# Optimization experiments

Measured on AMD Instinct MI355X. Metric: run time of the kernel, lower is better.

## Reference

```python
import jax, jax.numpy as jnp
import numpy as np

D_MODEL = 1024
D_INNER = 2048
D_STATE = 16
D_CONV = 4
DT_RANK = 64
BATCH = 2
SEQLEN = 1024


def setup_inputs() -> dict:
    key = jax.random.key(0)
    ks = jax.random.split(key, 12)
    s = 0.02
    # dt bias initialized as inverse-softplus of dt ~ LogUniform(1e-3, 1e-1), as in the torch code
    dt = jnp.exp(jax.random.uniform(ks[7], (D_INNER,)) * (np.log(0.1) - np.log(0.001)) + np.log(0.001))
    dt = jnp.clip(dt, 1e-4, None)
    inv_dt = jnp.log(jnp.expm1(dt))
    A_log = jnp.log(jnp.broadcast_to(jnp.arange(1, D_STATE + 1, dtype=jnp.float32), (D_INNER, D_STATE)))
    return {
        "hidden_states": jax.random.normal(ks[0], (BATCH, SEQLEN, D_MODEL), jnp.float32),
        "x_text": jax.random.normal(ks[1], (BATCH, D_MODEL), jnp.float32),
        "in_proj_w": jax.random.normal(ks[2], (2 * D_INNER, D_MODEL), jnp.float32) * s,
        "conv_w": jax.random.normal(ks[3], (D_INNER, 1, D_CONV), jnp.float32) * s,
        "conv_b": jax.random.normal(ks[4], (D_INNER,), jnp.float32) * s,
        "x_proj_w": jax.random.normal(ks[5], (DT_RANK + 2 * D_STATE, D_INNER), jnp.float32) * s,
        "dt_proj_w": jax.random.normal(ks[6], (D_INNER, DT_RANK), jnp.float32) * (DT_RANK ** -0.5),
        "dt_proj_b": inv_dt.astype(jnp.float32),
        "A_log": A_log.astype(jnp.float32),
        "D": jnp.ones((D_INNER,), jnp.float32),
        "out_proj_w": jax.random.normal(ks[8], (D_MODEL, D_INNER), jnp.float32) * s,
        "gate_w": jax.random.normal(ks[9], (DT_RANK + 2 * D_STATE, D_MODEL), jnp.float32) * s,
        "gate_b": jnp.zeros((DT_RANK + 2 * D_STATE,), jnp.float32),
    }


def _causal_depthwise_conv(x, w, b):
    # x: (b, d, l), w: (d, 1, k) depthwise, left-pad k-1 for causality
    y = jax.lax.conv_general_dilated(
        x, w, window_strides=(1,), padding=[(D_CONV - 1, 0)],
        dimension_numbers=("NCH", "OIH", "NCH"), feature_group_count=D_INNER)
    return y + b[None, :, None]


def _mamba_forward(hidden_states, x_text, in_proj_w, conv_w, conv_b, x_proj_w,
                   dt_proj_w, dt_proj_b, A_log, D, out_proj_w, gate_w, gate_b):
    b = hidden_states.shape[0]
    # input projection -> x, z each (b, l, d_inner)
    xz = jnp.einsum("bld,ed->ble", hidden_states, in_proj_w)
    x, z = jnp.split(xz, 2, axis=-1)
    # causal depthwise conv + SiLU
    xc = _causal_depthwise_conv(jnp.transpose(x, (0, 2, 1)), conv_w, conv_b)
    xc = jnp.transpose(jax.nn.silu(xc), (0, 2, 1))  # (b, l, d_inner)
    # x_proj -> dt/B/C, modulated by text gate
    x_dbl = jnp.einsum("bld,ed->ble", xc, x_proj_w)  # (b, l, dt_rank+2n)
    gate = jax.nn.sigmoid(x_text @ gate_w.T + gate_b)  # (b, dt_rank+2n)
    x_dbl = x_dbl * gate[:, None, :]
    dt, Bm, Cm = jnp.split(x_dbl, [DT_RANK, DT_RANK + D_STATE], axis=-1)
    delta = jax.nn.softplus(jnp.einsum("blr,dr->bld", dt, dt_proj_w) + dt_proj_b)  # (b, l, d)
    A = -jnp.exp(A_log)  # (d, n)
    dA = jnp.exp(jnp.einsum("bld,dn->bldn", delta, A))          # (b, l, d, n)
    dBx = jnp.einsum("bld,bln->bldn", delta * xc, Bm)            # (b, l, d, n)

    def step(h, inp):
        dA_t, dBx_t, C_t = inp
        h = h * dA_t + dBx_t                       # (b, d, n)
        y_t = jnp.einsum("bdn,bn->bd", h, C_t)
        return h, y_t

    h0 = jnp.zeros((b, D_INNER, D_STATE), delta.dtype)
    _, ys = jax.lax.scan(step, h0, (jnp.transpose(dA, (1, 0, 2, 3)),
                                    jnp.transpose(dBx, (1, 0, 2, 3)),
                                    jnp.transpose(Cm, (1, 0, 2))))
    y = jnp.transpose(ys, (1, 0, 2)) + D * xc      # (b, l, d_inner)
    y = y * jax.nn.silu(z)
    return jnp.einsum("bld,md->blm", y, out_proj_w)


def reference(hidden_states, x_text, in_proj_w, conv_w, conv_b, x_proj_w,
              dt_proj_w, dt_proj_b, A_log, D, out_proj_w, gate_w, gate_b):
    return _mamba_forward(hidden_states, x_text, in_proj_w, conv_w, conv_b, x_proj_w,
                          dt_proj_w, dt_proj_b, A_log, D, out_proj_w, gate_w, gate_b)
```

## Files before the change

### kernel.cpp

```cpp
#include <hip/hip_runtime.h>

#define BATCH   2
#define SEQLEN  1024
#define DMODEL  1024
#define DINNER  2048
#define DSTATE  16
#define DCONV   4
#define DTRANK  64
#define GDIM    96
#define MROWS   (BATCH*SEQLEN)

#define NCHUNK  64
#define LCHUNK  16
#define SPLITX  16
#define SPLITO  2

typedef __attribute__((ext_vector_type(8))) short bf16x8_t;
typedef __attribute__((ext_vector_type(4))) float f32x4_t;
typedef __attribute__((ext_vector_type(4))) unsigned short u16x4_t;
typedef unsigned short ushort_t;

__device__ __forceinline__ unsigned short f2bf(float x) {
    union { float f; unsigned int u; } v; v.f = x;
    unsigned int r = v.u + 0x7FFFu + ((v.u >> 16) & 1u);
    return (unsigned short)(r >> 16);
}
__device__ __forceinline__ float bf2f(unsigned short h) {
    union { unsigned int u; float f; } v; v.u = ((unsigned int)h) << 16;
    return v.f;
}

__device__ __forceinline__ void gload_lds16(const ushort_t* g, short* l) {
    __builtin_amdgcn_global_load_lds(
        (const __attribute__((address_space(1))) unsigned int*)g,
        (__attribute__((address_space(3))) unsigned int*)l, 16, 0, 0);
}

#define N1 (MROWS*DMODEL)
#define N2 (2*DINNER*DMODEL)
#define N3 (GDIM*DINNER)
#define N4 (DINNER*DTRANK)
#define N5 (DMODEL*DINNER)
#define NTOT (N1+N2+N3+N4+N5)
__global__ __launch_bounds__(256)
void cvt5_kernel(const float* __restrict__ s1, const float* __restrict__ s2,
                 const float* __restrict__ s3, const float* __restrict__ s4,
                 const float* __restrict__ s5,
                 ushort_t* o1, ushort_t* o2, ushort_t* o3, ushort_t* o4, ushort_t* o5) {
    int idx = (blockIdx.x * 256 + threadIdx.x) * 4;
    if (idx >= NTOT) return;
    const float* src; ushort_t* dst;
    if (idx < N1)              { src = s1; dst = o1; }
    else if ((idx -= N1) < N2) { src = s2; dst = o2; }
    else if ((idx -= N2) < N3) { src = s3; dst = o3; }
    else if ((idx -= N3) < N4) { src = s4; dst = o4; }
    else                       { idx -= N4; src = s5; dst = o5; }
    f32x4_t v = *(const f32x4_t*)(src + idx);
    u16x4_t o;
    #pragma unroll
    for (int j = 0; j < 4; j++) o[j] = f2bf(v[j]);
    *(u16x4_t*)(dst + idx) = o;
}

template<int EPI>
__global__ __launch_bounds__(256)
void gemm_bf(const ushort_t* __restrict__ A, const ushort_t* __restrict__ W,
             void* __restrict__ out0, void* __restrict__ out1,
             const float* __restrict__ bias, int M, int N, int K) {
    __shared__ __align__(16) short As[2][128 * 32];
    __shared__ __align__(16) short Bs[2][128 * 32];

    const int tid  = threadIdx.x;
    const int m0   = blockIdx.x * 128;
    const int n0   = blockIdx.y * 128;
    const int klen = K / gridDim.z;
    const int kbeg = blockIdx.z * klen;

    const int w    = tid >> 6;
    const int lane = tid & 63;
    const int quad = lane >> 4;
    const int l15  = lane & 15;
    const int wm   = (w >> 1) * 64;
    const int wn   = (w & 1) * 64;

    const int rA0 = (w * 2 + 0) * 16 + (lane >> 2);
    const int rA1 = (w * 2 + 1) * 16 + (lane >> 2);
    const int kc  = (((lane & 3) ^ ((lane >> 3) & 3)) << 3);
    const int arow0 = m0 + rA0;
    const int arow1 = m0 + rA1;
    int brow0 = n0 + rA0; if (brow0 > N - 1) brow0 = N - 1;
    int brow1 = n0 + rA1; if (brow1 > N - 1) brow1 = N - 1;

    const int sw = ((quad ^ ((l15 >> 1) & 3)) << 3);

    f32x4_t acc[4][4];
    #pragma unroll
    for (int i = 0; i < 4; i++)
        #pragma unroll
        for (int j = 0; j < 4; j++)
            acc[i][j] = (f32x4_t){0.f, 0.f, 0.f, 0.f};

    {
        const int kk = kbeg + kc;
        gload_lds16(A + (size_t)arow0 * K + kk, &As[0][(w * 2 + 0) * 512]);
        gload_lds16(A + (size_t)arow1 * K + kk, &As[0][(w * 2 + 1) * 512]);
        gload_lds16(W + (size_t)brow0 * K + kk, &Bs[0][(w * 2 + 0) * 512]);
        gload_lds16(W + (size_t)brow1 * K + kk, &Bs[0][(w * 2 + 1) * 512]);
    }

    int cur = 0;
    for (int k0 = 0; k0 < klen; k0 += 32) {
        if (k0 + 32 < klen) {
            const int kk = kbeg + k0 + 32 + kc;
            gload_lds16(A + (size_t)arow0 * K + kk, &As[cur ^ 1][(w * 2 + 0) * 512]);
            gload_lds16(A + (size_t)arow1 * K + kk, &As[cur ^ 1][(w * 2 + 1) * 512]);
            gload_lds16(W + (size_t)brow0 * K + kk, &Bs[cur ^ 1][(w * 2 + 0) * 512]);
            gload_lds16(W + (size_t)brow1 * K + kk, &Bs[cur ^ 1][(w * 2 + 1) * 512]);
            asm volatile("s_waitcnt vmcnt(4)" ::: "memory");
        } else {
            asm volatile("s_waitcnt vmcnt(0)" ::: "memory");
        }
        __builtin_amdgcn_sched_barrier(0);
        asm volatile("s_barrier" ::: "memory");
        __builtin_amdgcn_sched_barrier(0);

        bf16x8_t af[4], bfv[4];
        #pragma unroll
        for (int mi = 0; mi < 4; mi++)
            af[mi] = *(const bf16x8_t*)(&As[cur][(wm + mi * 16 + l15) * 32 + sw]);
        #pragma unroll
        for (int ni = 0; ni < 4; ni++)
            bfv[ni] = *(const bf16x8_t*)(&Bs[cur][(wn + ni * 16 + l15) * 32 + sw]);
        #pragma unroll
        for (int mi = 0; mi < 4; mi++)
            #pragma unroll
            for (int ni = 0; ni < 4; ni++)
                acc[mi][ni] = __builtin_amdgcn_mfma_f32_16x16x32_bf16(af[mi], bfv[ni], acc[mi][ni], 0, 0, 0);

        __builtin_amdgcn_sched_barrier(0);
        asm volatile("s_barrier" ::: "memory");
        __builtin_amdgcn_sched_barrier(0);
        cur ^= 1;
    }

    const size_t zoff = (size_t)blockIdx.z * M * N;
    #pragma unroll
    for (int mi = 0; mi < 4; mi++) {
        #pragma unroll
        for (int ni = 0; ni < 4; ni++) {
            #pragma unroll
            for (int r = 0; r < 4; r++) {
                int gm = m0 + wm + mi * 16 + quad * 4 + r;
                int gn = n0 + wn + ni * 16 + l15;
                if (gn < N) {
                    float v = acc[mi][ni][r];
                    if (EPI == 0) {
                        ((float*)out0)[zoff + (size_t)gm * N + gn] = v;
                    } else if (EPI == 1) {
                        float t = v + bias[gn];
                        float sp = (t > 20.f) ? t : log1pf(__expf(t));
                        ((ushort_t*)out0)[(size_t)gm * N + gn] = f2bf(sp);
                    } else {
                        if (gn < DINNER)
                            ((float*)out0)[(size_t)gm * DINNER + gn] = v;
                        else
                            ((float*)out1)[(size_t)gm * DINNER + (gn - DINNER)] = v;
                    }
                }
            }
        }
    }
}

#define CONVBLK ((MROWS*DINNER)/256)
__global__ __launch_bounds__(256)
void convgate_kernel(const float* __restrict__ x,
                     const float* __restrict__ cw,
                     const float* __restrict__ cb,
                     ushort_t* __restrict__ xc,
                     const float* __restrict__ xt,
                     const float* __restrict__ gw,
                     const float* __restrict__ gb,
                     float* __restrict__ gate) {
    if (blockIdx.x < CONVBLK) {
        int idx = blockIdx.x * 256 + threadIdx.x;
        int d  = idx & (DINNER - 1);
        int bl = idx >> 11;
        int l  = bl & (SEQLEN - 1);
        float acc = cb[d];
        #pragma unroll
        for (int j = 0; j < DCONV; j++) {
            int lj = l - (DCONV - 1) + j;
            if (lj >= 0)
                acc += cw[d * DCONV + j] * x[(size_t)(bl - (DCONV - 1) + j) * DINNER + d];
        }
        float v = acc / (1.f + __expf(-acc));
        xc[idx] = f2bf(v);
    } else {
        int g = blockIdx.x - CONVBLK;
        int b = g / GDIM, j = g % GDIM;
        int tid = threadIdx.x;
        float s = 0.f;
        for (int k = tid; k < DMODEL; k += 256)
            s += xt[b * DMODEL + k] * gw[j * DMODEL + k];
        #pragma unroll
        for (int o = 32; o > 0; o >>= 1) s += __shfl_down(s, o);
        __shared__ float red[4];
        if ((tid & 63) == 0) red[tid >> 6] = s;
        __syncthreads();
        if (tid == 0) {
            float t = red[0] + red[1] + red[2] + red[3] + gb[j];
            gate[b * GDIM + j] = 1.f / (1.f + __expf(-t));
        }
    }
}

__global__ void gatemul_kernel(const float* __restrict__ xp,
                               const float* __restrict__ gate,
                               ushort_t* __restrict__ dt,
                               float* __restrict__ Bm,
                               float* __restrict__ Cm) {
    int idx = blockIdx.x * 256 + threadIdx.x;
    if (idx >= MROWS * GDIM) return;
    int j  = idx % GDIM;
    int bl = idx / GDIM;
    int b  = bl >> 10;
    float v = 0.f;
    #pragma unroll
    for (int z = 0; z < SPLITX; z++)
        v += xp[(size_t)z * MROWS * GDIM + idx];
    v *= gate[b * GDIM + j];
    if (j < DTRANK)               dt[bl * DTRANK + j] = f2bf(v);
    else if (j < DTRANK + DSTATE) Bm[bl * DSTATE + (j - DTRANK)] = v;
    else                          Cm[bl * DSTATE + (j - DTRANK - DSTATE)] = v;
}

__global__ __launch_bounds__(256)
void scan1_kernel(const ushort_t* __restrict__ delta,
                  const ushort_t* __restrict__ xc,
                  const float* __restrict__ Bm,
                  const float* __restrict__ A_log,
                  float* __restrict__ hfin,
                  float* __restrict__ dsum) {
    __shared__ float sBm[LCHUNK][DSTATE];
    int tid = threadIdx.x;
    int d = blockIdx.x * 256 + tid;
    int b = blockIdx.y;
    int c = blockIdx.z;
    int l0 = c * LCHUNK;
    for (int t = tid; t < LCHUNK * DSTATE; t += 256)
        sBm[t >> 4][t & 15] = Bm[((size_t)(b * SEQLEN + l0 + (t >> 4))) * DSTATE + (t & 15)];
    __syncthreads();

    float Ac[DSTATE];
    #pragma unroll
    for (int n = 0; n < DSTATE; n++)
        Ac[n] = -__expf(A_log[d * DSTATE + n]);
    float h[DSTATE];
    #pragma unroll
    for (int n = 0; n < DSTATE; n++) h[n] = 0.f;
    float ds = 0.f;

    for (int s = 0; s < LCHUNK; s++) {
        size_t ix = (size_t)(b * SEQLEN + l0 + s) * DINNER + d;
        float dv = bf2f(delta[ix]);
        float xv = bf2f(xc[ix]);
        float dx = dv * xv;
        ds += dv;
        #pragma unroll
        for (int n = 0; n < DSTATE; n++) {
            float e = __expf(dv * Ac[n]);
            h[n] = h[n] * e + dx * sBm[s][n];
        }
    }
    size_t base = ((size_t)(b * DINNER + d) * NCHUNK + c) * DSTATE;
    #pragma unroll
    for (int n = 0; n < DSTATE; n++) hfin[base + n] = h[n];
    dsum[((size_t)b * NCHUNK + c) * DINNER + d] = ds;
}

__global__ __launch_bounds__(256)
void scan2_kernel(float* __restrict__ hfin,
                  const float* __restrict__ dsum,
                  const float* __restrict__ A_log) {
    __shared__ float sh[NCHUNK * DSTATE];
    __shared__ float sp[NCHUNK * DSTATE];
    __shared__ float sAc[DSTATE];
    __shared__ float sds[NCHUNK];
    const int tid = threadIdx.x;
    const int bd  = blockIdx.x;
    const int b   = bd >> 11;
    const int d   = bd & (DINNER - 1);
    if (tid < DSTATE) sAc[tid] = -__expf(A_log[d * DSTATE + tid]);
    if (tid < NCHUNK) sds[tid] = dsum[((size_t)b * NCHUNK + tid) * DINNER + d];
    const size_t base = (size_t)bd * (NCHUNK * DSTATE);
    float hl[4];
    #pragma unroll
    for (int r = 0; r < 4; r++) hl[r] = hfin[base + tid + r * 256];
    __syncthreads();
    #pragma unroll
    for (int r = 0; r < 4; r++) {
        int i = tid + r * 256;
        sh[i] = hl[r];
        sp[i] = __expf(sAc[i & 15] * sds[i >> 4]);
    }
    __syncthreads();
    #pragma unroll
    for (int s = 1; s < NCHUNK; s <<= 1) {
        float nh[4], np[4];
        #pragma unroll
        for (int r = 0; r < 4; r++) {
            int i = tid + r * 256;
            int c = i >> 4;
            if (c >= s) {
                int j = i - (s << 4);
                nh[r] = sh[i] + sp[i] * sh[j];
                np[r] = sp[i] * sp[j];
            } else { nh[r] = sh[i]; np[r] = sp[i]; }
        }
        __syncthreads();
        #pragma unroll
        for (int r = 0; r < 4; r++) { int i = tid + r * 256; sh[i] = nh[r]; sp[i] = np[r]; }
        __syncthreads();
    }
    #pragma unroll
    for (int r = 0; r < 4; r++) {
        int i = tid + r * 256;
        hfin[base + i] = (i >> 4) ? sh[i - 16] : 0.f;
    }
}

__global__ __launch_bounds__(256)
void scan3_kernel(const ushort_t* __restrict__ delta,
                  ushort_t* __restrict__ xc,
                  const float* __restrict__ z,
                  const float* __restrict__ Bm,
                  const float* __restrict__ Cm,
                  const float* __restrict__ A_log,
                  const float* __restrict__ Dp,
                  const float* __restrict__ h0) {
    __shared__ float sBm[LCHUNK][DSTATE];
    __shared__ float sCm[LCHUNK][DSTATE];
    int tid = threadIdx.x;
    int d = blockIdx.x * 256 + tid;
    int b = blockIdx.y;
    int c = blockIdx.z;
    int l0 = c * LCHUNK;
    for (int t = tid; t < LCHUNK * DSTATE; t += 256) {
        size_t src = ((size_t)(b * SEQLEN + l0 + (t >> 4))) * DSTATE + (t & 15);
        sBm[t >> 4][t & 15] = Bm[src];
        sCm[t >> 4][t & 15] = Cm[src];
    }
    __syncthreads();

    float Ac[DSTATE];
    #pragma unroll
    for (int n = 0; n < DSTATE; n++)
        Ac[n] = -__expf(A_log[d * DSTATE + n]);

    float h[DSTATE];
    size_t hb0 = ((size_t)(b * DINNER + d) * NCHUNK + c) * DSTATE;
    #pragma unroll
    for (int n = 0; n < DSTATE; n++) h[n] = h0[hb0 + n];

    float Dv = Dp[d];

    for (int s = 0; s < LCHUNK; s++) {
        size_t ix = (size_t)(b * SEQLEN + l0 + s) * DINNER + d;
        float dv = bf2f(delta[ix]);
        float xv = bf2f(xc[ix]);
        float dx = dv * xv;
        float y = 0.f;
        #pragma unroll
        for (int n = 0; n < DSTATE; n++) {
            float e = __expf(dv * Ac[n]);
            h[n] = h[n] * e + dx * sBm[s][n];
            y += h[n] * sCm[s][n];
        }
        float zv = z[ix];
        float o = (y + Dv * xv) * (zv / (1.f + __expf(-zv)));
        xc[ix] = f2bf(o);
    }
}

__global__ void reduce2_kernel(const float* __restrict__ p, float* __restrict__ out, int n) {
    int i = blockIdx.x * 256 + threadIdx.x;
    if (i < n)
        out[i] = p[i] + p[(size_t)n + i];
}

extern "C" void kernel_launch(void* const* d_in, const int* in_sizes, int n_in,
                              void* d_out, int out_size, void* d_ws, size_t ws_size,
                              hipStream_t stream) {
    const float* hidden   = (const float*)d_in[0];
    const float* x_text   = (const float*)d_in[1];
    const float* in_proj  = (const float*)d_in[2];
    const float* conv_w   = (const float*)d_in[3];
    const float* conv_b   = (const float*)d_in[4];
    const float* x_proj   = (const float*)d_in[5];
    const float* dt_proj  = (const float*)d_in[6];
    const float* dt_bias  = (const float*)d_in[7];
    const float* A_log    = (const float*)d_in[8];
    const float* Dparam   = (const float*)d_in[9];
    const float* out_proj = (const float*)d_in[10];
    const float* gate_w   = (const float*)d_in[11];
    const float* gate_b   = (const float*)d_in[12];

    char* ws = (char*)d_ws;
    size_t off = 0;
    auto alloc = [&](size_t bytes) -> char* {
        char* p = ws + off;
        off += (bytes + 255) & ~(size_t)255;
        return p;
    };
    ushort_t* hb    = (ushort_t*)alloc((size_t)N1 * 2);
    ushort_t* w_in  = (ushort_t*)alloc((size_t)N2 * 2);
    ushort_t* w_x   = (ushort_t*)alloc((size_t)N3 * 2);
    ushort_t* w_dt  = (ushort_t*)alloc((size_t)N4 * 2);
    ushort_t* w_o   = (ushort_t*)alloc((size_t)N5 * 2);
    float*    X     = (float*)alloc((size_t)MROWS * DINNER * 4);
    float*    zbuf  = (float*)alloc((size_t)MROWS * DINNER * 4);
    float*    xpart = (float*)alloc((size_t)SPLITX * MROWS * GDIM * 4);
    float*    hfin2 = (float*)alloc((size_t)BATCH * DINNER * NCHUNK * DSTATE * 4 - (size_t)SPLITX * MROWS * GDIM * 4);
    float*    dsum  = (float*)alloc((size_t)BATCH * NCHUNK * DINNER * 4);
    float*    gate  = (float*)alloc((size_t)BATCH * GDIM * 4);
    float*    Bm    = (float*)alloc((size_t)MROWS * DSTATE * 4);
    float*    Cm    = (float*)alloc((size_t)MROWS * DSTATE * 4);
    ushort_t* dt    = (ushort_t*)alloc((size_t)MROWS * DTRANK * 2);
    (void)hfin2;

    ushort_t* xc    = w_in;
    ushort_t* delta = (ushort_t*)X;
    float*    hfin  = xpart;
    float*    outp  = X;

    cvt5_kernel<<<(NTOT / 4 + 255) / 256, 256, 0, stream>>>(
        hidden, in_proj, x_proj, dt_proj, out_proj, hb, w_in, w_x, w_dt, w_o);

    gemm_bf<3><<<dim3(MROWS / 128, (2 * DINNER) / 128, 1), 256, 0, stream>>>(
        hb, w_in, X, zbuf, nullptr, MROWS, 2 * DINNER, DMODEL);

    convgate_kernel<<<CONVBLK + BATCH * GDIM, 256, 0, stream>>>(
        X, conv_w, conv_b, xc, x_text, gate_w, gate_b, gate);

    gemm_bf<0><<<dim3(MROWS / 128, 1, SPLITX), 256, 0, stream>>>(
        xc, w_x, xpart, nullptr, nullptr, MROWS, GDIM, DINNER);

    gatemul_kernel<<<(MROWS * GDIM + 255) / 256, 256, 0, stream>>>(
        xpart, gate, dt, Bm, Cm);

    gemm_bf<1><<<dim3(MROWS / 128, DINNER / 128, 1), 256, 0, stream>>>(
        dt, w_dt, delta, nullptr, dt_bias, MROWS, DINNER, DTRANK);

    scan1_kernel<<<dim3(DINNER / 256, BATCH, NCHUNK), 256, 0, stream>>>(
        delta, xc, Bm, A_log, hfin, dsum);

    scan2_kernel<<<BATCH * DINNER, 256, 0, stream>>>(hfin, dsum, A_log);

    scan3_kernel<<<dim3(DINNER / 256, BATCH, NCHUNK), 256, 0, stream>>>(
        delta, xc, zbuf, Bm, Cm, A_log, Dparam, hfin);

    gemm_bf<0><<<dim3(MROWS / 128, DMODEL / 128, SPLITO), 256, 0, stream>>>(
        xc, w_o, outp, nullptr, nullptr, MROWS, DMODEL, DINNER);

    reduce2_kernel<<<(MROWS * DMODEL + 255) / 256, 256, 0, stream>>>(
        outp, (float*)d_out, MROWS * DMODEL);
}
```

Measured before the change: 281.5 us.

## Fuse chunk-scan pass into dt_proj GEMM and drop out_proj split-K reduction

Moves the first chunked-scan pass (per-chunk state and delta sum) into the epilogue of the dt_proj GEMM, which removes one kernel launch and re-reads delta through cache right after writing it. The output projection now uses a narrower 128x64 tile template (NF=2) with no split-K and writes straight to the output, removing the partial-sum buffer and the reduce kernel. The fused epilogue runs a serial 16-step scan per thread inside the GEMM blocks, which may raise register pressure and lower occupancy. The workspace layout is also simplified.

```diff
diff --git a/kernel.cpp b/kernel.cpp
--- a/kernel.cpp
+++ b/kernel.cpp
@@ -13,7 +13,6 @@
 #define NCHUNK  64
 #define LCHUNK  16
 #define SPLITX  16
-#define SPLITO  2
 
 typedef __attribute__((ext_vector_type(8))) short bf16x8_t;
 typedef __attribute__((ext_vector_type(4))) float f32x4_t;
@@ -62,17 +61,20 @@
     *(u16x4_t*)(dst + idx) = o;
 }
 
-template<int EPI>
+template<int EPI, int NF>
 __global__ __launch_bounds__(256)
 void gemm_bf(const ushort_t* __restrict__ A, const ushort_t* __restrict__ W,
              void* __restrict__ out0, void* __restrict__ out1,
-             const float* __restrict__ bias, int M, int N, int K) {
+             const float* __restrict__ bias, int M, int N, int K,
+             const ushort_t* __restrict__ xcp, const float* __restrict__ Bmp,
+             const float* __restrict__ A_logp, float* __restrict__ hfinp,
+             float* __restrict__ dsump) {
     __shared__ __align__(16) short As[2][128 * 32];
-    __shared__ __align__(16) short Bs[2][128 * 32];
+    __shared__ __align__(16) short Bs[2][(NF * 32) * 32];
 
     const int tid  = threadIdx.x;
     const int m0   = blockIdx.x * 128;
-    const int n0   = blockIdx.y * 128;
+    const int n0   = blockIdx.y * (NF * 32);
     const int klen = K / gridDim.z;
     const int kbeg = blockIdx.z * klen;
 
@@ -81,31 +83,32 @@
     const int quad = lane >> 4;
     const int l15  = lane & 15;
     const int wm   = (w >> 1) * 64;
-    const int wn   = (w & 1) * 64;
-
-    const int rA0 = (w * 2 + 0) * 16 + (lane >> 2);
-    const int rA1 = (w * 2 + 1) * 16 + (lane >> 2);
+    const int wn   = (w & 1) * (NF * 16);
+
+    const int rl  = lane >> 2;
     const int kc  = (((lane & 3) ^ ((lane >> 3) & 3)) << 3);
-    const int arow0 = m0 + rA0;
-    const int arow1 = m0 + rA1;
-    int brow0 = n0 + rA0; if (brow0 > N - 1) brow0 = N - 1;
-    int brow1 = n0 + rA1; if (brow1 > N - 1) brow1 = N - 1;
+    const int arow0 = m0 + (w * 2 + 0) * 16 + rl;
+    const int arow1 = m0 + (w * 2 + 1) * 16 + rl;
+    int brow0 = n0 + (w * (NF / 2) + 0) * 16 + rl; if (brow0 > N - 1) brow0 = N - 1;
+    int brow1 = 0;
+    if constexpr (NF == 4) { brow1 = n0 + (w * 2 + 1) * 16 + rl; if (brow1 > N - 1) brow1 = N - 1; }
 
     const int sw = ((quad ^ ((l15 >> 1) & 3)) << 3);
 
-    f32x4_t acc[4][4];
+    f32x4_t acc[4][NF];
     #pragma unroll
     for (int i = 0; i < 4; i++)
         #pragma unroll
-        for (int j = 0; j < 4; j++)
+        for (int j = 0; j < NF; j++)
             acc[i][j] = (f32x4_t){0.f, 0.f, 0.f, 0.f};
 
     {
         const int kk = kbeg + kc;
         gload_lds16(A + (size_t)arow0 * K + kk, &As[0][(w * 2 + 0) * 512]);
         gload_lds16(A + (size_t)arow1 * K + kk, &As[0][(w * 2 + 1) * 512]);
-        gload_lds16(W + (size_t)brow0 * K + kk, &Bs[0][(w * 2 + 0) * 512]);
-        gload_lds16(W + (size_t)brow1 * K + kk, &Bs[0][(w * 2 + 1) * 512]);
+        gload_lds16(W + (size_t)brow0 * K + kk, &Bs[0][(w * (NF / 2) + 0) * 512]);
+        if constexpr (NF == 4)
+            gload_lds16(W + (size_t)brow1 * K + kk, &Bs[0][(w * 2 + 1) * 512]);
     }
 
     int cur = 0;
@@ -114,9 +117,11 @@
             const int kk = kbeg + k0 + 32 + kc;
             gload_lds16(A + (size_t)arow0 * K + kk, &As[cur ^ 1][(w * 2 + 0) * 512]);
             gload_lds16(A + (size_t)arow1 * K + kk, &As[cur ^ 1][(w * 2 + 1) * 512]);
-            gload_lds16(W + (size_t)brow0 * K + kk, &Bs[cur ^ 1][(w * 2 + 0) * 512]);
-            gload_lds16(W + (size_t)brow1 * K + kk, &Bs[cur ^ 1][(w * 2 + 1) * 512]);
-            asm volatile("s_waitcnt vmcnt(4)" ::: "memory");
+            gload_lds16(W + (size_t)brow0 * K + kk, &Bs[cur ^ 1][(w * (NF / 2) + 0) * 512]);
+            if constexpr (NF == 4)
+                gload_lds16(W + (size_t)brow1 * K + kk, &Bs[cur ^ 1][(w * 2 + 1) * 512]);
+            if constexpr (NF == 4) asm volatile("s_waitcnt vmcnt(4)" ::: "memory");
+            else                   asm volatile("s_waitcnt vmcnt(3)" ::: "memory");
         } else {
             asm volatile("s_waitcnt vmcnt(0)" ::: "memory");
         }
@@ -124,17 +129,17 @@
         asm volatile("s_barrier" ::: "memory");
         __builtin_amdgcn_sched_barrier(0);
 
-        bf16x8_t af[4], bfv[4];
+        bf16x8_t af[4], bfv[NF];
         #pragma unroll
         for (int mi = 0; mi < 4; mi++)
             af[mi] = *(const bf16x8_t*)(&As[cur][(wm + mi * 16 + l15) * 32 + sw]);
         #pragma unroll
-        for (int ni = 0; ni < 4; ni++)
+        for (int ni = 0; ni < NF; ni++)
             bfv[ni] = *(const bf16x8_t*)(&Bs[cur][(wn + ni * 16 + l15) * 32 + sw]);
         #pragma unroll
         for (int mi = 0; mi < 4; mi++)
             #pragma unroll
-            for (int ni = 0; ni < 4; ni++)
+            for (int ni = 0; ni < NF; ni++)
                 acc[mi][ni] = __builtin_amdgcn_mfma_f32_16x16x32_bf16(af[mi], bfv[ni], acc[mi][ni], 0, 0, 0);
 
         __builtin_amdgcn_sched_barrier(0);
@@ -147,7 +152,7 @@
     #pragma unroll
     for (int mi = 0; mi < 4; mi++) {
         #pragma unroll
-        for (int ni = 0; ni < 4; ni++) {
+        for (int ni = 0; ni < NF; ni++) {
             #pragma unroll
             for (int r = 0; r < 4; r++) {
                 int gm = m0 + wm + mi * 16 + quad * 4 + r;
@@ -156,18 +161,64 @@
                     float v = acc[mi][ni][r];
                     if (EPI == 0) {
                         ((float*)out0)[zoff + (size_t)gm * N + gn] = v;
-                    } else if (EPI == 1) {
+                    } else if (EPI == 2) {
                         float t = v + bias[gn];
                         float sp = (t > 20.f) ? t : log1pf(__expf(t));
                         ((ushort_t*)out0)[(size_t)gm * N + gn] = f2bf(sp);
-                    } else {
+                    } else if (EPI == 3) {
                         if (gn < DINNER)
                             ((float*)out0)[(size_t)gm * DINNER + gn] = v;
                         else
                             ((float*)out1)[(size_t)gm * DINNER + (gn - DINNER)] = v;
+                    } else {
+                        ((float*)out0)[(size_t)gm * N + gn] = v;
                     }
                 }
             }
+        }
+    }
+
+    if constexpr (EPI == 2) {
+        __shared__ float sBm[128][DSTATE];
+        for (int t = tid; t < 128 * DSTATE; t += 256)
+            sBm[t >> 4][t & 15] = Bmp[((size_t)m0 + (t >> 4)) * DSTATE + (t & 15)];
+        __syncthreads();
+
+        const ushort_t* dg = (const ushort_t*)out0;
+        const int col = tid & 127;
+        const int d   = n0 + col;
+        const int b   = m0 >> 10;
+        const int c0g = (m0 & 1023) >> 4;
+        float Ac[DSTATE];
+        #pragma unroll
+        for (int n = 0; n < DSTATE; n++)
+            Ac[n] = -__expf(A_logp[(size_t)d * DSTATE + n]);
+
+        #pragma unroll
+        for (int cc = 0; cc < 4; cc++) {
+            const int c_loc = (tid >> 7) * 4 + cc;
+            float h[DSTATE];
+            #pragma unroll
+            for (int n = 0; n < DSTATE; n++) h[n] = 0.f;
+            float ds = 0.f;
+            for (int s = 0; s < LCHUNK; s++) {
+                const int lr = c_loc * LCHUNK + s;
+                const size_t ix = (size_t)(m0 + lr) * DINNER + d;
+                float dv = bf2f(dg[ix]);
+                float xv = bf2f(xcp[ix]);
+                float dx = dv * xv;
+                ds += dv;
+                #pragma unroll
+                for (int n = 0; n < DSTATE; n++) {
+                    float e = __expf(dv * Ac[n]);
+                    h[n] = h[n] * e + dx * sBm[lr][n];
+                }
+            }
+            const int cg = c0g + c_loc;
+            size_t base = ((size_t)(b * DINNER + d) * NCHUNK + cg) * DSTATE;
+            #pragma unroll
+            for (int n = 0; n < DSTATE; n++) hfinp[base + n] = h[n];
+            dsump[((size_t)b * NCHUNK + cg) * DINNER + d] = ds;
         }
     }
 }
@@ -233,50 +284,6 @@
     if (j < DTRANK)               dt[bl * DTRANK + j] = f2bf(v);
     else if (j < DTRANK + DSTATE) Bm[bl * DSTATE + (j - DTRANK)] = v;
     else                          Cm[bl * DSTATE + (j - DTRANK - DSTATE)] = v;
-}
-
-__global__ __launch_bounds__(256)
-void scan1_kernel(const ushort_t* __restrict__ delta,
-                  const ushort_t* __restrict__ xc,
-                  const float* __restrict__ Bm,
-                  const float* __restrict__ A_log,
-                  float* __restrict__ hfin,
-                  float* __restrict__ dsum) {
-    __shared__ float sBm[LCHUNK][DSTATE];
-    int tid = threadIdx.x;
-    int d = blockIdx.x * 256 + tid;
-    int b = blockIdx.y;
-    int c = blockIdx.z;
-    int l0 = c * LCHUNK;
-    for (int t = tid; t < LCHUNK * DSTATE; t += 256)
-        sBm[t >> 4][t & 15] = Bm[((size_t)(b * SEQLEN + l0 + (t >> 4))) * DSTATE + (t & 15)];
-    __syncthreads();
-
-    float Ac[DSTATE];
-    #pragma unroll
-    for (int n = 0; n < DSTATE; n++)
-        Ac[n] = -__expf(A_log[d * DSTATE + n]);
-    float h[DSTATE];
-    #pragma unroll
-    for (int n = 0; n < DSTATE; n++) h[n] = 0.f;
-    float ds = 0.f;
-
-    for (int s = 0; s < LCHUNK; s++) {
-        size_t ix = (size_t)(b * SEQLEN + l0 + s) * DINNER + d;
-        float dv = bf2f(delta[ix]);
-        float xv = bf2f(xc[ix]);
-        float dx = dv * xv;
-        ds += dv;
-        #pragma unroll
-        for (int n = 0; n < DSTATE; n++) {
-            float e = __expf(dv * Ac[n]);
-            h[n] = h[n] * e + dx * sBm[s][n];
-        }
-    }
-    size_t base = ((size_t)(b * DINNER + d) * NCHUNK + c) * DSTATE;
-    #pragma unroll
-    for (int n = 0; n < DSTATE; n++) hfin[base + n] = h[n];
-    dsum[((size_t)b * NCHUNK + c) * DINNER + d] = ds;
 }
 
 __global__ __launch_bounds__(256)
@@ -383,12 +390,6 @@
     }
 }
 
-__global__ void reduce2_kernel(const float* __restrict__ p, float* __restrict__ out, int n) {
-    int i = blockIdx.x * 256 + threadIdx.x;
-    if (i < n)
-        out[i] = p[i] + p[(size_t)n + i];
-}
-
 extern "C" void kernel_launch(void* const* d_in, const int* in_sizes, int n_in,
                               void* d_out, int out_size, void* d_ws, size_t ws_size,
                               hipStream_t stream) {
@@ -420,49 +421,44 @@
     ushort_t* w_o   = (ushort_t*)alloc((size_t)N5 * 2);
     float*    X     = (float*)alloc((size_t)MROWS * DINNER * 4);
     float*    zbuf  = (float*)alloc((size_t)MROWS * DINNER * 4);
-    float*    xpart = (float*)alloc((size_t)SPLITX * MROWS * GDIM * 4);
-    float*    hfin2 = (float*)alloc((size_t)BATCH * DINNER * NCHUNK * DSTATE * 4 - (size_t)SPLITX * MROWS * GDIM * 4);
+    float*    hfin  = (float*)alloc((size_t)BATCH * DINNER * NCHUNK * DSTATE * 4);
     float*    dsum  = (float*)alloc((size_t)BATCH * NCHUNK * DINNER * 4);
     float*    gate  = (float*)alloc((size_t)BATCH * GDIM * 4);
     float*    Bm    = (float*)alloc((size_t)MROWS * DSTATE * 4);
     float*    Cm    = (float*)alloc((size_t)MROWS * DSTATE * 4);
     ushort_t* dt    = (ushort_t*)alloc((size_t)MROWS * DTRANK * 2);
-    (void)hfin2;
 
     ushort_t* xc    = w_in;
     ushort_t* delta = (ushort_t*)X;
-    float*    hfin  = xpart;
-    float*    outp  = X;
+    float*    xpart = hfin;
 
     cvt5_kernel<<<(NTOT / 4 + 255) / 256, 256, 0, stream>>>(
         hidden, in_proj, x_proj, dt_proj, out_proj, hb, w_in, w_x, w_dt, w_o);
 
-    gemm_bf<3><<<dim3(MROWS / 128, (2 * DINNER) / 128, 1), 256, 0, stream>>>(
-        hb, w_in, X, zbuf, nullptr, MROWS, 2 * DINNER, DMODEL);
+    gemm_bf<3, 4><<<dim3(MROWS / 128, (2 * DINNER) / 128, 1), 256, 0, stream>>>(
+        hb, w_in, X, zbuf, nullptr, MROWS, 2 * DINNER, DMODEL,
+        nullptr, nullptr, nullptr, nullptr, nullptr);
 
     convgate_kernel<<<CONVBLK + BATCH * GDIM, 256, 0, stream>>>(
         X, conv_w, conv_b, xc, x_text, gate_w, gate_b, gate);
 
-    gemm_bf<0><<<dim3(MROWS / 128, 1, SPLITX), 256, 0, stream>>>(
-        xc, w_x, xpart, nullptr, nullptr, MROWS, GDIM, DINNER);
+    gemm_bf<0, 4><<<dim3(MROWS / 128, 1, SPLITX), 256, 0, stream>>>(
+        xc, w_x, xpart, nullptr, nullptr, MROWS, GDIM, DINNER,
+        nullptr, nullptr, nullptr, nullptr, nullptr);
 
     gatemul_kernel<<<(MROWS * GDIM + 255) / 256, 256, 0, stream>>>(
         xpart, gate, dt, Bm, Cm);
 
-    gemm_bf<1><<<dim3(MROWS / 128, DINNER / 128, 1), 256, 0, stream>>>(
-        dt, w_dt, delta, nullptr, dt_bias, MROWS, DINNER, DTRANK);
-
-    scan1_kernel<<<dim3(DINNER / 256, BATCH, NCHUNK), 256, 0, stream>>>(
-        delta, xc, Bm, A_log, hfin, dsum);
+    gemm_bf<2, 4><<<dim3(MROWS / 128, DINNER / 128, 1), 256, 0, stream>>>(
+        dt, w_dt, delta, nullptr, dt_bias, MROWS, DINNER, DTRANK,
+        xc, Bm, A_log, hfin, dsum);
 
     scan2_kernel<<<BATCH * DINNER, 256, 0, stream>>>(hfin, dsum, A_log);
 
     scan3_kernel<<<dim3(DINNER / 256, BATCH, NCHUNK), 256, 0, stream>>>(
         delta, xc, zbuf, Bm, Cm, A_log, Dparam, hfin);
 
-    gemm_bf<0><<<dim3(MROWS / 128, DMODEL / 128, SPLITO), 256, 0, stream>>>(
-        xc, w_o, outp, nullptr, nullptr, MROWS, DMODEL, DINNER);
-
-    reduce2_kernel<<<(MROWS * DMODEL + 255) / 256, 256, 0, stream>>>(
-        outp, (float*)d_out, MROWS * DMODEL);
-}
+    gemm_bf<5, 2><<<dim3(MROWS / 128, DMODEL / 64, 1), 256, 0, stream>>>(
+        xc, w_o, (float*)d_out, nullptr, nullptr, MROWS, DMODEL, DINNER,
+        nullptr, nullptr, nullptr, nullptr, nullptr);
+}
```

After: 299.7 us. 6.5% more time.
